# Kernel optimization log

Measured on AMD Instinct MI355X. Metric: run time of the kernel, lower is better.

Reference implementation:

```python
import jax, jax.numpy as jnp
import numpy as np

RADII = [2, 4]
EPS = 1e-6


def _avg_pool_hw(t, k):
    # valid avg-pool with kernel k, stride 1 over the last two dims
    nd = t.ndim
    win = (1,) * (nd - 2) + (k, k)
    s = jax.lax.reduce_window(t, 0.0, jax.lax.add, win, (1,) * nd, 'VALID')
    return s / float(k * k)


def _patch_cca(x, y, r):
    B, C1, H, W = x.shape
    C2 = y.shape[1]
    k = 2 * r + 1
    pad = ((0, 0), (0, 0), (r, r), (r, r))
    xp = jnp.pad(x, pad, mode='reflect')  # (B,C1,Hp,Wp)
    yp = jnp.pad(y, pad, mode='reflect')  # (B,C2,Hp,Wp)

    # local second moments via outer products + avg pooling
    xx = _avg_pool_hw(xp[:, :, None] * xp[:, None], k)  # (B,C1,C1,H,W)
    yy = _avg_pool_hw(yp[:, :, None] * yp[:, None], k)  # (B,C2,C2,H,W)
    xy = _avg_pool_hw(xp[:, :, None] * yp[:, None], k)  # (B,C1,C2,H,W)
    xm = _avg_pool_hw(xp, k)  # (B,C1,H,W)
    ym = _avg_pool_hw(yp, k)  # (B,C2,H,W)

    cxx = xx - xm[:, :, None] * xm[:, None]
    cyy = yy - ym[:, :, None] * ym[:, None]
    cxy = xy - xm[:, :, None] * ym[:, None]

    # move matrix dims last: (B,H,W,Ci,Cj)
    cxx = jnp.transpose(cxx, (0, 3, 4, 1, 2)) + EPS * jnp.eye(C1, dtype=x.dtype)
    cyy = jnp.transpose(cyy, (0, 3, 4, 1, 2)) + EPS * jnp.eye(C2, dtype=x.dtype)
    cxy = jnp.transpose(cxy, (0, 3, 4, 1, 2))

    lx_inv = jnp.linalg.inv(jnp.linalg.cholesky(cxx))  # (B,H,W,C1,C1)
    ly_inv = jnp.linalg.inv(jnp.linalg.cholesky(cyy))  # (B,H,W,C2,C2)
    corr = jnp.einsum('bhwij,bhwjk,bhwkl->bhwil', lx_inv, cxy, ly_inv)
    diag = jnp.diagonal(corr, axis1=-2, axis2=-1)  # (B,H,W,min(C1,C2))
    sim = jnp.abs(diag).sum(-1) / min(C1, C2)  # (B,H,W)
    return sim[:, None]  # (B,1,H,W)


def setup_inputs() -> dict:
    key = jax.random.key(0)
    kx, ky = jax.random.split(key)
    B, C, H, W = 2, 6, 512, 512
    x = jax.random.normal(kx, (B, C, H, W), dtype=jnp.float32)
    y = jax.random.normal(ky, (B, C, H, W), dtype=jnp.float32)
    return {'x': x, 'y': y}


def reference(x, y):
    # stack per-radius CCA maps on a trailing axis -> (B,1,H,W,len(RADII))
    return jnp.stack([_patch_cca(x, y, r) for r in RADII], axis=-1)
```

## Files before the change

kernel.cpp:

```cpp
#include <hip/hip_runtime.h>
#include <math.h>

typedef float v2f __attribute__((ext_vector_type(2)));
typedef float v4f __attribute__((ext_vector_type(4)));

#define LT(i,j) ((i)*((i)+1)/2 + (j))

__device__ __forceinline__ int reflect512(int i) {
  int a = (i < 0) ? -i : i;
  int b = 1022 - a;
  return (a < b) ? a : b;
}

__device__ __forceinline__ float gget(const v2f* accd, const v2f* accs,
                                      int a, int b) {
  const int t = LT(a >> 1, b >> 1);
  if (((a & 1) == 0) && ((b & 1) == 0)) return accd[t].x;
  if (((a & 1) == 1) && ((b & 1) == 1)) return accd[t].y;
  if ((a & 1) == 0) return accs[t].x;
  return accs[t].y;
}

__device__ __forceinline__ void cholinv6(float* a) {
  #pragma unroll
  for (int j = 0; j < 6; ++j) {
    float d = a[LT(j,j)];
    #pragma unroll
    for (int p = 0; p < j; ++p) d -= a[LT(j,p)] * a[LT(j,p)];
    const float rd = __builtin_amdgcn_rsqf(d);
    a[LT(j,j)] = rd;
    #pragma unroll
    for (int i = j + 1; i < 6; ++i) {
      float s = a[LT(i,j)];
      #pragma unroll
      for (int p = 0; p < j; ++p) s -= a[LT(i,p)] * a[LT(j,p)];
      a[LT(i,j)] = s * rd;
    }
  }
  #pragma unroll
  for (int j = 0; j < 6; ++j) {
    #pragma unroll
    for (int i = j + 1; i < 6; ++i) {
      float s = 0.0f;
      #pragma unroll
      for (int p = j; p < i; ++p) s += a[LT(i,p)] * a[LT(p,j)];
      a[LT(i,j)] = -s * a[LT(i,i)];
    }
  }
}

template <int K, bool ADD>
__device__ __forceinline__ void row_acc_pk(const float* __restrict__ ls,
                                           int rowbase,
                                           v2f* zs, v2f* accd, v2f* accs) {
  #pragma unroll
  for (int dx = 0; dx < K; ++dx) {
    const v4f l0 = *(const v4f*)&ls[rowbase + dx * 12 + 0];
    const v4f l1 = *(const v4f*)&ls[rowbase + dx * 12 + 4];
    const v4f l2 = *(const v4f*)&ls[rowbase + dx * 12 + 8];
    v2f z[6];
    z[0] = l0.lo; z[1] = l0.hi;
    z[2] = l1.lo; z[3] = l1.hi;
    z[4] = l2.lo; z[5] = l2.hi;
    #pragma unroll
    for (int p = 0; p < 6; ++p) zs[p] = ADD ? (zs[p] + z[p]) : (zs[p] - z[p]);
    int t = 0;
    #pragma unroll
    for (int Kp = 0; Kp < 6; ++Kp) {
      #pragma unroll
      for (int Pp = 0; Pp <= Kp; ++Pp) {
        const v2f c  = z[Pp];
        const v2f cs = __builtin_shufflevector(c, c, 1, 0);
        const v2f a  = ADD ? z[Kp] : -z[Kp];
        accd[t] = __builtin_elementwise_fma(a, c,  accd[t]);
        accs[t] = __builtin_elementwise_fma(a, cs, accs[t]);
        ++t;
      }
    }
  }
}

template <int K>
__device__ __forceinline__ float emit_sim(const v2f* zs, const v2f* accd,
                                          const v2f* accs) {
  constexpr float inv_n = 1.0f / (K * K);
  float mx[6], my[6];
  #pragma unroll
  for (int i = 0; i < 6; ++i) {
    mx[i] = ((i & 1) ? zs[i >> 1].y : zs[i >> 1].x) * inv_n;
    my[i] = ((i & 1) ? zs[3 + (i >> 1)].y : zs[3 + (i >> 1)].x) * inv_n;
  }
  float ax[21];
  {
    int t = 0;
    #pragma unroll
    for (int i = 0; i < 6; ++i)
      #pragma unroll
      for (int j = 0; j <= i; ++j) {
        const float e = (i == j) ? 1e-6f : 0.0f;
        ax[t] = gget(accd, accs, i, j) * inv_n - mx[i] * mx[j] + e;
        ++t;
      }
  }
  cholinv6(ax);
  float ay[21];
  {
    int t = 0;
    #pragma unroll
    for (int i = 0; i < 6; ++i)
      #pragma unroll
      for (int j = 0; j <= i; ++j) {
        const float e = (i == j) ? 1e-6f : 0.0f;
        ay[t] = gget(accd, accs, 6 + i, 6 + j) * inv_n - my[i] * my[j] + e;
        ++t;
      }
  }
  cholinv6(ay);
  float cxy[36];
  #pragma unroll
  for (int i = 0; i < 6; ++i)
    #pragma unroll
    for (int j = 0; j < 6; ++j)
      cxy[i * 6 + j] = fmaf(-mx[i], my[j], gget(accd, accs, 6 + j, i) * inv_n);
  float sim = 0.0f;
  #pragma unroll
  for (int i = 0; i < 6; ++i) {
    float di = 0.0f;
    #pragma unroll
    for (int j = 0; j <= i; ++j) {
      float inner = 0.0f;
      #pragma unroll
      for (int k = i; k < 6; ++k) inner += cxy[j * 6 + k] * ay[LT(k, i)];
      di += ax[LT(i, j)] * inner;
    }
    sim += fabsf(di);
  }
  return sim * (1.0f / 6.0f);
}

template <int R, int V>
__global__ __launch_bounds__(256, 2)
void cca_slide_pk(const float* __restrict__ xg, const float* __restrict__ yg,
                  float* __restrict__ out, const int ri) {
  constexpr int H = 512, W = 512, HW = H * W;
  constexpr int K = 2 * R + 1;
  constexpr int TW = 16;
  constexpr int TH = 16 * V;
  constexpr int SW = TW + 2 * R;
  constexpr int SH = TH + 2 * R;

  __shared__ __align__(16) float ls[SH * SW * 12];

  const int b   = blockIdx.z;
  const int h0  = blockIdx.y * TH;
  const int w0  = blockIdx.x * TW;
  const int tid = threadIdx.x;

  for (int i = tid; i < SH * SW; i += 256) {
    const int row = i / SW;
    const int col = i - row * SW;
    const int h = reflect512(h0 - R + row);
    const int w = reflect512(w0 - R + col);
    const size_t gp = (size_t)b * 6 * HW + (size_t)h * W + w;
    float xv[6], yv[6];
    #pragma unroll
    for (int c = 0; c < 6; ++c) {
      xv[c] = xg[gp + c * HW];
      yv[c] = yg[gp + c * HW];
    }
    v4f p0 = {xv[0], xv[1], xv[2], xv[3]};
    v4f p1 = {xv[4], xv[5], yv[0], yv[1]};
    v4f p2 = {yv[2], yv[3], yv[4], yv[5]};
    *(v4f*)&ls[i * 12 + 0] = p0;
    *(v4f*)&ls[i * 12 + 4] = p1;
    *(v4f*)&ls[i * 12 + 8] = p2;
  }
  __syncthreads();

  const int tx = tid & 15;
  const int g  = tid >> 4;
  const int r0 = g * V;

  v2f zs[6]    = {};
  v2f accd[21] = {};
  v2f accs[21] = {};

  #pragma unroll 1
  for (int dy = 0; dy < K; ++dy)
    row_acc_pk<K, true>(ls, ((r0 + dy) * SW + tx) * 12, zs, accd, accs);

  out[((size_t)((b * H + h0 + r0) * W + w0 + tx)) * 2 + ri] =
      emit_sim<K>(zs, accd, accs);

  #pragma unroll 1
  for (int s = 1; s < V; ++s) {
    row_acc_pk<K, true >(ls, ((r0 + s + 2 * R) * SW + tx) * 12, zs, accd, accs);
    row_acc_pk<K, false>(ls, ((r0 + s - 1)     * SW + tx) * 12, zs, accd, accs);
    out[((size_t)((b * H + h0 + r0 + s) * W + w0 + tx)) * 2 + ri] =
        emit_sim<K>(zs, accd, accs);
  }
}

extern "C" void kernel_launch(void* const* d_in, const int* in_sizes, int n_in,
                              void* d_out, int out_size, void* d_ws, size_t ws_size,
                              hipStream_t stream) {
  const float* x = (const float*)d_in[0];
  const float* y = (const float*)d_in[1];
  float* out = (float*)d_out;
  constexpr int V = 2;
  dim3 grid(512 / 16, 512 / (16 * V), 2);
  cca_slide_pk<2, V><<<grid, dim3(256), 0, stream>>>(x, y, out, 0);
  cca_slide_pk<4, V><<<grid, dim3(256), 0, stream>>>(x, y, out, 1);
}
```

Measured before the change: 151.4 us.

## Pre-interleave padded inputs into workspace and read directly from global memory

Adds a prep kernel that writes a reflect-padded, channel-interleaved copy of x and y (12 floats per pixel) to the workspace. The main kernel drops its LDS tile staging and syncthreads and reads each pixel's 12 values from global memory as vector loads, relying on the cache for reuse. It also merges both radii into one launch through blockIdx.z and raises the rows processed per thread from 2 to 8, which cuts redundant window rebuilds in the sliding sum. The cost is an extra pass over the inputs, roughly 26 MB of workspace traffic, and heavier per-load latency in place of LDS reads.

Measured after the change: 137.2 us. 9.4% less time.

```diff
diff --git a/kernel.cpp b/kernel.cpp
--- a/kernel.cpp
+++ b/kernel.cpp
@@ -10,6 +10,38 @@
   int a = (i < 0) ? -i : i;
   int b = 1022 - a;
   return (a < b) ? a : b;
+}
+
+constexpr int HB  = 520;
+constexpr int PS  = 12;
+constexpr int RS  = HB * PS;
+
+__global__ __launch_bounds__(256)
+void prep_interleave(const float* __restrict__ xg, const float* __restrict__ yg,
+                     float* __restrict__ zb) {
+  constexpr int H = 512, W = 512, HW = H * W;
+  const int idx = blockIdx.x * 256 + threadIdx.x;
+  if (idx >= 2 * HB * HB) return;
+  const int b  = idx / (HB * HB);
+  const int r2 = idx - b * (HB * HB);
+  const int hr = r2 / HB;
+  const int wc = r2 - hr * HB;
+  const int h = reflect512(hr - 4);
+  const int w = reflect512(wc - 4);
+  const size_t gp = (size_t)b * 6 * HW + (size_t)h * W + w;
+  float xv[6], yv[6];
+  #pragma unroll
+  for (int c = 0; c < 6; ++c) {
+    xv[c] = xg[gp + c * HW];
+    yv[c] = yg[gp + c * HW];
+  }
+  float* o = zb + (size_t)idx * PS;
+  v4f p0 = {xv[0], xv[1], xv[2], xv[3]};
+  v4f p1 = {xv[4], xv[5], yv[0], yv[1]};
+  v4f p2 = {yv[2], yv[3], yv[4], yv[5]};
+  *(v4f*)(o + 0) = p0;
+  *(v4f*)(o + 4) = p1;
+  *(v4f*)(o + 8) = p2;
 }
 
 __device__ __forceinline__ float gget(const v2f* accd, const v2f* accs,
@@ -50,20 +82,19 @@
 }
 
 template <int K, bool ADD>
-__device__ __forceinline__ void row_acc_pk(const float* __restrict__ ls,
-                                           int rowbase,
-                                           v2f* zs, v2f* accd, v2f* accs) {
+__device__ __forceinline__ void row_acc_g(const float* __restrict__ p,
+                                          v2f* zs, v2f* accd, v2f* accs) {
   #pragma unroll
   for (int dx = 0; dx < K; ++dx) {
-    const v4f l0 = *(const v4f*)&ls[rowbase + dx * 12 + 0];
-    const v4f l1 = *(const v4f*)&ls[rowbase + dx * 12 + 4];
-    const v4f l2 = *(const v4f*)&ls[rowbase + dx * 12 + 8];
+    const v4f l0 = *(const v4f*)(p + dx * PS + 0);
+    const v4f l1 = *(const v4f*)(p + dx * PS + 4);
+    const v4f l2 = *(const v4f*)(p + dx * PS + 8);
     v2f z[6];
     z[0] = l0.lo; z[1] = l0.hi;
     z[2] = l1.lo; z[3] = l1.hi;
     z[4] = l2.lo; z[5] = l2.hi;
     #pragma unroll
-    for (int p = 0; p < 6; ++p) zs[p] = ADD ? (zs[p] + z[p]) : (zs[p] - z[p]);
+    for (int q = 0; q < 6; ++q) zs[q] = ADD ? (zs[q] + z[q]) : (zs[q] - z[q]);
     int t = 0;
     #pragma unroll
     for (int Kp = 0; Kp < 6; ++Kp) {
@@ -139,47 +170,20 @@
 }
 
 template <int R, int V>
-__global__ __launch_bounds__(256, 2)
-void cca_slide_pk(const float* __restrict__ xg, const float* __restrict__ yg,
-                  float* __restrict__ out, const int ri) {
-  constexpr int H = 512, W = 512, HW = H * W;
+__device__ __forceinline__ void run(const float* __restrict__ zb,
+                                    float* __restrict__ out, int b, int ri) {
   constexpr int K = 2 * R + 1;
-  constexpr int TW = 16;
-  constexpr int TH = 16 * V;
-  constexpr int SW = TW + 2 * R;
-  constexpr int SH = TH + 2 * R;
-
-  __shared__ __align__(16) float ls[SH * SW * 12];
-
-  const int b   = blockIdx.z;
-  const int h0  = blockIdx.y * TH;
-  const int w0  = blockIdx.x * TW;
-  const int tid = threadIdx.x;
-
-  for (int i = tid; i < SH * SW; i += 256) {
-    const int row = i / SW;
-    const int col = i - row * SW;
-    const int h = reflect512(h0 - R + row);
-    const int w = reflect512(w0 - R + col);
-    const size_t gp = (size_t)b * 6 * HW + (size_t)h * W + w;
-    float xv[6], yv[6];
-    #pragma unroll
-    for (int c = 0; c < 6; ++c) {
-      xv[c] = xg[gp + c * HW];
-      yv[c] = yg[gp + c * HW];
-    }
-    v4f p0 = {xv[0], xv[1], xv[2], xv[3]};
-    v4f p1 = {xv[4], xv[5], yv[0], yv[1]};
-    v4f p2 = {yv[2], yv[3], yv[4], yv[5]};
-    *(v4f*)&ls[i * 12 + 0] = p0;
-    *(v4f*)&ls[i * 12 + 4] = p1;
-    *(v4f*)&ls[i * 12 + 8] = p2;
-  }
-  __syncthreads();
-
-  const int tx = tid & 15;
-  const int g  = tid >> 4;
-  const int r0 = g * V;
+  constexpr int H = 512, W = 512;
+
+  const int h0 = blockIdx.y * (16 * V);
+  const int w0 = blockIdx.x * 16;
+  const int tx = threadIdx.x & 15;
+  const int g  = threadIdx.x >> 4;
+  const int hbase = h0 + g * V;
+  const int wc = w0 + tx;
+
+  const float* base = zb + (size_t)b * HB * RS
+                    + (size_t)(hbase + 4 - R) * RS + (size_t)(wc + 4 - R) * PS;
 
   v2f zs[6]    = {};
   v2f accd[21] = {};
@@ -187,18 +191,25 @@
 
   #pragma unroll 1
   for (int dy = 0; dy < K; ++dy)
-    row_acc_pk<K, true>(ls, ((r0 + dy) * SW + tx) * 12, zs, accd, accs);
-
-  out[((size_t)((b * H + h0 + r0) * W + w0 + tx)) * 2 + ri] =
+    row_acc_g<K, true>(base + dy * RS, zs, accd, accs);
+
+  out[((size_t)((b * H + hbase) * W + wc)) * 2 + ri] =
       emit_sim<K>(zs, accd, accs);
 
   #pragma unroll 1
   for (int s = 1; s < V; ++s) {
-    row_acc_pk<K, true >(ls, ((r0 + s + 2 * R) * SW + tx) * 12, zs, accd, accs);
-    row_acc_pk<K, false>(ls, ((r0 + s - 1)     * SW + tx) * 12, zs, accd, accs);
-    out[((size_t)((b * H + h0 + r0 + s) * W + w0 + tx)) * 2 + ri] =
+    row_acc_g<K, true >(base + (s + 2 * R) * RS, zs, accd, accs);
+    row_acc_g<K, false>(base + (s - 1)     * RS, zs, accd, accs);
+    out[((size_t)((b * H + hbase + s) * W + wc)) * 2 + ri] =
         emit_sim<K>(zs, accd, accs);
   }
+}
+
+__global__ __launch_bounds__(256, 2)
+void cca_v8(const float* __restrict__ zb, float* __restrict__ out) {
+  const int z = blockIdx.z;
+  if (z < 2) run<2, 8>(zb, out, z, 0);
+  else       run<4, 8>(zb, out, z - 2, 1);
 }
 
 extern "C" void kernel_launch(void* const* d_in, const int* in_sizes, int n_in,
@@ -207,8 +218,12 @@
   const float* x = (const float*)d_in[0];
   const float* y = (const float*)d_in[1];
   float* out = (float*)d_out;
-  constexpr int V = 2;
-  dim3 grid(512 / 16, 512 / (16 * V), 2);
-  cca_slide_pk<2, V><<<grid, dim3(256), 0, stream>>>(x, y, out, 0);
-  cca_slide_pk<4, V><<<grid, dim3(256), 0, stream>>>(x, y, out, 1);
-}
+  float* zb  = (float*)d_ws;
+
+  {
+    const int n = 2 * HB * HB;
+    prep_interleave<<<dim3((n + 255) / 256), dim3(256), 0, stream>>>(x, y, zb);
+  }
+  dim3 grid(512 / 16, 512 / (16 * 8), 4);
+  cca_v8<<<grid, dim3(256), 0, stream>>>(zb, out);
+}
```
